# Performance work log

Hardware: AMD Instinct MI355X
Metric: run time of the kernel (lower is better)

## Reference

```python
import jax, jax.numpy as jnp
import numpy as np

STEPS = 100
RATE = 200
THR = 1.0
BETA = 0.0
SG_ALPHA = 2.0  # snntorch default ATan surrogate alpha


@jax.custom_vjp
def spike_fn(x):
    # heaviside spike with atan surrogate gradient (snntorch default)
    return (x > 0).astype(x.dtype)

def _spike_fwd(x):
    return spike_fn(x), x

def _spike_bwd(x, g):
    grad = (SG_ALPHA / 2.0) / (1.0 + (jnp.pi / 2.0 * SG_ALPHA * x) ** 2)
    return (g * grad,)

spike_fn.defvjp(_spike_fwd, _spike_bwd)


def conv2d(x, w):
    # x: [B,C,H,W], w: [O,I,K,K], VALID, stride 1, no bias
    return jax.lax.conv_general_dilated(
        x, w, window_strides=(1, 1), padding='VALID',
        dimension_numbers=('NCHW', 'OIHW', 'NCHW'))


def avg_pool2(x):
    s = jax.lax.reduce_window(x, 0.0, jax.lax.add, (1, 1, 2, 2), (1, 1, 2, 2), 'VALID')
    return s * 0.25


def lif(cur, mem):
    # snntorch Leaky, reset_mechanism='subtract'; reset signal is detached
    reset = jax.lax.stop_gradient((mem > THR).astype(cur.dtype))
    mem = BETA * mem + cur - reset * THR
    spk = spike_fn(mem - THR)
    return spk, mem


def setup_inputs() -> dict:
    key = jax.random.key(0)
    k1, k2, k3, k4 = jax.random.split(key, 4)
    B, C, H, W = 64, 3, 32, 32
    x = jax.random.uniform(k1, (B, C, H, W), dtype=jnp.float32)
    # kaiming-uniform-ish init scales (exact values irrelevant for correctness baseline)
    W_in = jax.random.normal(k2, (32, 3, 5, 5), dtype=jnp.float32) * 0.1
    W_h1 = jax.random.normal(k3, (64, 32, 5, 5), dtype=jnp.float32) * 0.05
    W_h2 = jax.random.normal(k4, (10, 1600), dtype=jnp.float32) * 0.02
    return {"x": x, "W_in": W_in, "W_h1": W_h1, "W_h2": W_h2}


def reference(x, W_in, W_h1, W_h2):
    B, C, H, W = x.shape
    K = W_in.shape[2]
    # poisson spike train: [steps, B, C, H, W]
    rescale = RATE / STEPS
    rand = jax.random.uniform(jax.random.key(1), (STEPS, B, C, H, W), dtype=x.dtype)
    spikes = (rand < x * rescale).astype(x.dtype)

    H1 = (H - K + 1) // 2; W1 = (W - K + 1) // 2           # after conv1+pool
    H2 = (H1 - K + 1) // 2; W2 = (W1 - K + 1) // 2          # after conv2+pool
    mem0 = (jnp.zeros((B, W_in.shape[0], H1, W1), x.dtype),
            jnp.zeros((B, W_h1.shape[0], H2, W2), x.dtype),
            jnp.zeros((B, W_h2.shape[0]), x.dtype))

    def step(carry, s):
        memin, memh1, memh2 = carry
        spkin, memin = lif(avg_pool2(conv2d(s, W_in)), memin)
        spkh1, memh1 = lif(avg_pool2(conv2d(spkin, W_h1)), memh1)
        flat = spkh1.reshape(spkh1.shape[0], -1)
        spkh2, memh2 = lif(flat @ W_h2.T, memh2)
        return (memin, memh1, memh2), (spkh2, memh2)

    _, (out_spikes, memh2_mem) = jax.lax.scan(step, mem0, spikes)
    return out_spikes, memh2_mem
```

## Files before the change

kernel.cpp:

```cpp
#include <hip/hip_runtime.h>
#include <stdint.h>


#define NSTEPS 100
#define NB 64
#define CAPF1 524288u
#define CAPF2 262144u

typedef short bf16x8 __attribute__((ext_vector_type(8)));
typedef float f32x4 __attribute__((ext_vector_type(4)));

__device__ __forceinline__ uint32_t rotl32(uint32_t v, uint32_t r) {
  return (v << r) | (v >> (32u - r));
}

__device__ __forceinline__ void threefry2x32(uint32_t k0, uint32_t k1,
                                             uint32_t& x0, uint32_t& x1) {
  uint32_t k2 = k0 ^ k1 ^ 0x1BD11BDAu;
  x0 += k0; x1 += k1;
#define TF_R(r) { x0 += x1; x1 = rotl32(x1, r); x1 ^= x0; }
  TF_R(13u) TF_R(15u) TF_R(26u) TF_R(6u)
  x0 += k1; x1 += k2 + 1u;
  TF_R(17u) TF_R(29u) TF_R(16u) TF_R(24u)
  x0 += k2; x1 += k0 + 2u;
  TF_R(13u) TF_R(15u) TF_R(26u) TF_R(6u)
  x0 += k0; x1 += k1 + 3u;
  TF_R(17u) TF_R(29u) TF_R(16u) TF_R(24u)
  x0 += k1; x1 += k2 + 4u;
  TF_R(13u) TF_R(15u) TF_R(26u) TF_R(6u)
  x0 += k2; x1 += k0 + 5u;
#undef TF_R
}

__device__ __forceinline__ double fold_pool_w(const float* W, int base, int pos) {
  int iy = pos / 6, ix = pos % 6;
  double w = 0.0;
  for (int dy = 0; dy < 2; ++dy) {
    int ky = iy - dy; if (ky < 0 || ky > 4) continue;
    for (int dx = 0; dx < 2; ++dx) {
      int kx = ix - dx; if (kx < 0 || kx > 4) continue;
      w += (double)W[base + ky * 5 + kx];
    }
  }
  return w;
}

__device__ __forceinline__ uint16_t f2bf(float x) {
  uint32_t u = __float_as_uint(x);
  uint32_t r = (u + 0x7fffu + ((u >> 16) & 1u)) >> 16;
  return (uint16_t)r;
}

__global__ __launch_bounds__(256) void prep_gen(const float* __restrict__ W_in,
                                                const float* __restrict__ W_h1,
                                                const float* __restrict__ x,
                                                double* __restrict__ W1R,
                                                double* __restrict__ W2R,
                                                uint16_t* __restrict__ WB1,
                                                uint16_t* __restrict__ WB2,
                                                float* __restrict__ EPS,
                                                uint32_t* __restrict__ cnt,
                                                uint32_t* __restrict__ rowm) {
  if (blockIdx.x >= 678) {
    int id = (blockIdx.x - 678) * 4 + (threadIdx.x >> 6);
    int lane = threadIdx.x & 63;
    int rp = id & 15, c = (id >> 4) % 3, tb = id / 48;
    int pix = rp * 64 + lane;
    int b = tb & 63;
    uint32_t i = (uint32_t)((tb * 3 + c) * 1024 + pix);
    uint32_t x0 = 0u, x1 = i;
    threefry2x32(0u, 1u, x0, x1);
    uint32_t bits = x0 ^ x1;
    float u = __uint_as_float((bits >> 9) | 0x3f800000u) - 1.0f;
    float xv = x[(b * 3 + c) * 1024 + pix];
    unsigned long long mask = __ballot(u < 2.0f * xv);
    if (lane == 0) ((unsigned long long*)rowm)[id] = mask;
    return;
  }
  if (blockIdx.x < 654) {
    int e = blockIdx.x * 256 + threadIdx.x;
    if (e < 3456) {
      int oj = e & 7, c = (e >> 3) % 3, pos = ((e >> 3) / 3) % 36, og = (e >> 3) / 108;
      int oc = og * 8 + oj;
      W1R[e] = fold_pool_w(W_in, (oc * 3 + c) * 25, pos);
    } else if (e < 77184) {
      int e2 = e - 3456;
      int oj = e2 & 15, pos = (e2 >> 4) % 36, c = ((e2 >> 4) / 36) % 32, og = e2 / 18432;
      int oc = og * 16 + oj;
      W2R[e2] = fold_pool_w(W_h1, (oc * 32 + c) * 25, pos);
    } else if (e < 93568) {
      int e3 = e - 77184;
      int j = e3 & 7, lane = (e3 >> 3) & 63, nt = (e3 >> 9) & 1, ks = (e3 >> 10) & 3, hl = e3 >> 12;
      int k = ks * 32 + (lane >> 4) * 8 + j;
      int oc = nt * 16 + (lane & 15);
      uint16_t val = 0;
      if (k < 108) {
        int c = k / 36, pos = k % 36;
        double w = fold_pool_w(W_in, (oc * 3 + c) * 25, pos);
        uint16_t hi = f2bf((float)w);
        if (hl == 0) val = hi;
        else {
          float hif = __uint_as_float(((uint32_t)hi) << 16);
          val = f2bf((float)(w - (double)hif));
        }
      }
      WB1[e3] = val;
    } else if (e < 167296) {
      int e4 = e - 93568;
      int j = e4 & 7, lane = (e4 >> 3) & 63, nt = (e4 >> 9) & 3, pos = e4 >> 11;
      int oc = nt * 16 + (lane & 15);
      int c  = (lane >> 4) * 8 + j;
      double w = fold_pool_w(W_h1, (oc * 32 + c) * 25, pos);
      uint16_t hi = f2bf((float)w);
      float hif = __uint_as_float(((uint32_t)hi) << 16);
      uint16_t lo = f2bf((float)(w - (double)hif));
      WB2[e4] = hi;
      WB2[73728 + e4] = lo;
    } else if (e < 167298) {
      cnt[e - 167296] = 0;
    }
  } else {
    int wid = threadIdx.x >> 6, lane = threadIdx.x & 63;
    int o = (blockIdx.x - 654) * 4 + wid;
    const double u24 = 5.9604644775390625e-08;
    double s = 0.0;
    if (o < 32) {
      for (int t = lane; t < 108; t += 64) {
        int pos = t / 3, c = t % 3;
        s += fabs(fold_pool_w(W_in, (o * 3 + c) * 25, pos));
      }
    } else {
      int oc = o - 32;
      for (int t = lane; t < 1152; t += 64) {
        int c = t / 36, pos = t % 36;
        s += fabs(fold_pool_w(W_h1, (oc * 32 + c) * 25, pos));
      }
    }
    #pragma unroll
    for (int off = 32; off > 0; off >>= 1) s += __shfl_xor(s, off);
    if (lane == 0)
      EPS[o] = (o < 32) ? (float)(s * (108.0 * u24 * 6.0) * 0.25)
                        : (float)(s * (1152.0 * u24 * 6.0) * 0.25);
  }
}

__global__ __launch_bounds__(256) void conv1_mfma(const uint32_t* __restrict__ rowm,
                                                  const uint16_t* __restrict__ WB1,
                                                  const float* __restrict__ EPS,
                                                  uint32_t* __restrict__ A1w,
                                                  uint32_t* __restrict__ B1w,
                                                  uint32_t* __restrict__ cnt,
                                                  uint32_t* __restrict__ list1) {
  __shared__ uint32_t sR[4][96];
  const int tid = threadIdx.x;
  const int wid = tid >> 6, lane = tid & 63;
  const int tb = blockIdx.x * 4 + wid;
  const int q = lane >> 4, ln = lane & 15;

  for (int i = lane; i < 96; i += 64) sR[wid][i] = rowm[tb * 96 + i];

  const float eps0 = EPS[ln];
  const float eps1 = EPS[16 + ln];

  bf16x8 bf[2][4][2];
  #pragma unroll
  for (int hl = 0; hl < 2; ++hl)
    #pragma unroll
    for (int ks = 0; ks < 4; ++ks)
      #pragma unroll
      for (int nt = 0; nt < 2; ++nt)
        bf[hl][ks][nt] =
            *(const bf16x8*)(WB1 + ((((hl * 4 + ks) * 2 + nt) * 64 + lane) * 8));

  const int wl = lane;
  const int qq = wl >> 2, rr = wl & 3;

  for (int mt = 0; mt < 13; ++mt) {
    int p = mt * 16 + ln;
    int pc = p < 196 ? p : 195;
    int oh = pc / 14, ow = pc % 14;
    uint64_t seg0 = 0, seg1 = 0, seg2 = 0;
    #pragma unroll
    for (int iy = 0; iy < 6; ++iy) {
      seg0 |= (uint64_t)((sR[wid][0 * 32 + 2 * oh + iy] >> (2 * ow)) & 0x3fu) << (6 * iy);
      seg1 |= (uint64_t)((sR[wid][1 * 32 + 2 * oh + iy] >> (2 * ow)) & 0x3fu) << (6 * iy);
      seg2 |= (uint64_t)((sR[wid][2 * 32 + 2 * oh + iy] >> (2 * ow)) & 0x3fu) << (6 * iy);
    }
    uint64_t lo = seg0 | (seg1 << 36);
    uint64_t hi = (seg1 >> 28) | (seg2 << 8);
    uint32_t wz[4] = {(uint32_t)lo, (uint32_t)(lo >> 32),
                      (uint32_t)hi, (uint32_t)(hi >> 32)};

    f32x4 acc0 = (f32x4)(0.0f), acc1 = (f32x4)(0.0f);
    #pragma unroll
    for (int ks = 0; ks < 4; ++ks) {
      uint32_t byte = (wz[ks] >> (q * 8)) & 0xffu;
      union { uint32_t u[4]; bf16x8 v; } a;
      #pragma unroll
      for (int i = 0; i < 4; ++i)
        a.u[i] = (((byte >> (2 * i)) & 1u) ? 0x3F80u : 0u) |
                 (((byte >> (2 * i + 1)) & 1u) ? 0x3F800000u : 0u);
      acc0 = __builtin_amdgcn_mfma_f32_16x16x32_bf16(a.v, bf[0][ks][0], acc0, 0, 0, 0);
      acc0 = __builtin_amdgcn_mfma_f32_16x16x32_bf16(a.v, bf[1][ks][0], acc0, 0, 0, 0);
      acc1 = __builtin_amdgcn_mfma_f32_16x16x32_bf16(a.v, bf[0][ks][1], acc1, 0, 0, 0);
      acc1 = __builtin_amdgcn_mfma_f32_16x16x32_bf16(a.v, bf[1][ks][1], acc1, 0, 0, 0);
    }

    unsigned long long bA0[4], bA1[4], bB0[4], bB1[4], bF0[4], bF1[4];
    #pragma unroll
    for (int r = 0; r < 4; ++r) {
      float c0 = acc0[r] * 0.25f;
      float c1 = acc1[r] * 0.25f;
      bA0[r] = __ballot(c0 > 1.0f);
      bB0[r] = __ballot(c0 > 2.0f);
      bF0[r] = __ballot(fabsf(c0 - 1.0f) <= eps0 || fabsf(c0 - 2.0f) <= eps0);
      bA1[r] = __ballot(c1 > 1.0f);
      bB1[r] = __ballot(c1 > 2.0f);
      bF1[r] = __ballot(fabsf(c1 - 1.0f) <= eps1 || fabsf(c1 - 2.0f) <= eps1);
    }

    int pw = mt * 16 + wl;
    if (wl < 16 && pw < 196) {
#define SEL(B) (rr == 0 ? B[0] : rr == 1 ? B[1] : rr == 2 ? B[2] : B[3])
      uint32_t wA = (uint32_t)((SEL(bA0) >> (qq * 16)) & 0xffffull) |
                    ((uint32_t)((SEL(bA1) >> (qq * 16)) & 0xffffull) << 16);
      uint32_t wB = (uint32_t)((SEL(bB0) >> (qq * 16)) & 0xffffull) |
                    ((uint32_t)((SEL(bB1) >> (qq * 16)) & 0xffffull) << 16);
      uint32_t wF = (uint32_t)((SEL(bF0) >> (qq * 16)) & 0xffffull) |
                    ((uint32_t)((SEL(bF1) >> (qq * 16)) & 0xffffull) << 16);
#undef SEL
      uint32_t idx = (uint32_t)(tb * 196 + pw);
      A1w[idx] = wA;
      B1w[idx] = wB;
      if (wF) {
        uint32_t n = (uint32_t)__popc(wF);
        uint32_t slot = atomicAdd(&cnt[0], n);
        uint32_t base = idx * 32u;
        while (wF) {
          int bit = __ffs(wF) - 1; wF &= wF - 1;
          if (slot < CAPF1) list1[slot] = base + (uint32_t)bit;
          ++slot;
        }
      }
    }
  }
}

__global__ __launch_bounds__(256) void fix1c(const uint32_t* __restrict__ cnt,
                                             const uint32_t* __restrict__ list,
                                             const uint32_t* __restrict__ rowm,
                                             const double* __restrict__ W1R,
                                             uint32_t* __restrict__ A1w,
                                             uint32_t* __restrict__ B1w) {
  uint32_t total = cnt[0]; if (total > CAPF1) total = CAPF1;
  const uint32_t g = blockIdx.x * 32 + (threadIdx.x >> 3);
  const int l = threadIdx.x & 7;
  const uint32_t gstride = gridDim.x * 32;
  for (uint32_t i = g; i < total; i += gstride) {
    uint32_t e = list[i];
    uint32_t x = e >> 5;
    int oc = (int)(e & 31u);
    int tb = (int)(x / 196), p = (int)(x % 196);
    int oh = p / 14, ow = p % 14;
    int og = oc >> 3, oj = oc & 7;
    const uint32_t* R = rowm + (size_t)tb * 96;
    double acc = 0.0;
    for (int t = l; t < 108; t += 8) {
      int pos = t / 3, c = t - pos * 3;
      int iy = pos / 6, ix = pos - iy * 6;
      double bd = (double)((R[c * 32 + 2 * oh + iy] >> (2 * ow + ix)) & 1u);
      acc = fma(bd, W1R[og * 864 + pos * 24 + c * 8 + oj], acc);
    }
    acc += __shfl_xor(acc, 1);
    acc += __shfl_xor(acc, 2);
    acc += __shfl_xor(acc, 4);
    if (l == 0) {
      float cur = (float)(acc * 0.25);
      uint32_t m = 1u << oc;
      if (cur > 1.0f) atomicOr(&A1w[x], m); else atomicAnd(&A1w[x], ~m);
      if (cur > 2.0f) atomicOr(&B1w[x], m); else atomicAnd(&B1w[x], ~m);
    }
  }
}

__global__ __launch_bounds__(64) void scan1(const uint32_t* __restrict__ A1w,
                                            const uint32_t* __restrict__ B1w,
                                            uint32_t* __restrict__ mask1) {
  int chain = blockIdx.x * 64 + threadIdx.x;
  if (chain >= NB * 196) return;
  int b = chain / 196, p = chain % 196;
  const size_t stride = (size_t)NB * 196;
  size_t base = (size_t)b * 196 + p;
  uint32_t prev = 0;
  #pragma unroll
  for (int seg = 0; seg < 4; ++seg) {
    uint32_t Abuf[25], Bbuf[25];
    size_t sb = base + (size_t)(seg * 25) * stride;
    #pragma unroll
    for (int i = 0; i < 25; ++i) {
      Abuf[i] = A1w[sb + i * stride];
      Bbuf[i] = B1w[sb + i * stride];
    }
    #pragma unroll
    for (int i = 0; i < 25; ++i) {
      uint32_t s = (Abuf[i] & ~prev) | (Bbuf[i] & prev);
      mask1[sb + i * stride] = s;
      prev = s;
    }
  }
}

#define CONV2_EPILOG(ACC, TBV)                                                \
  {                                                                           \
    const int w = lane;                                                       \
    const int pw = w >> 1, hfw = w & 1;                                       \
    _Pragma("unroll")                                                         \
    for (int mt2 = 0; mt2 < 2; ++mt2) {                                       \
      const int pt = pw - mt2 * 16;                                           \
      const bool wvalid = (w < 50) && (pt >= 0) && (pt < 16) && (pw < 25);    \
      const int qw = (pt & 15) >> 2, rw = pt & 3;                             \
      uint32_t wA = 0, wB = 0, wF = 0;                                        \
      _Pragma("unroll")                                                       \
      for (int nt = 0; nt < 4; ++nt) {                                        \
        unsigned long long bA[4], bB[4], bF[4];                               \
        _Pragma("unroll")                                                     \
        for (int reg = 0; reg < 4; ++reg) {                                   \
          float c = ACC[mt2 * 4 + nt][reg] * 0.25f;                           \
          float e = epsv[nt];                                                 \
          bA[reg] = __ballot(c > 1.0f);                                       \
          bB[reg] = __ballot(c > 2.0f);                                       \
          bF[reg] = __ballot(fabsf(c - 1.0f) <= e || fabsf(c - 2.0f) <= e);   \
        }                                                                     \
        if (wvalid && (nt >> 1) == hfw) {                                     \
          const int sh = (nt & 1) * 16;                                       \
          unsigned long long sA = rw == 0 ? bA[0] : rw == 1 ? bA[1] : rw == 2 ? bA[2] : bA[3]; \
          unsigned long long sB = rw == 0 ? bB[0] : rw == 1 ? bB[1] : rw == 2 ? bB[2] : bB[3]; \
          unsigned long long sF = rw == 0 ? bF[0] : rw == 1 ? bF[1] : rw == 2 ? bF[2] : bF[3]; \
          wA |= (uint32_t)((sA >> (qw * 16)) & 0xffffull) << sh;              \
          wB |= (uint32_t)((sB >> (qw * 16)) & 0xffffull) << sh;              \
          wF |= (uint32_t)((sF >> (qw * 16)) & 0xffffull) << sh;              \
        }                                                                     \
      }                                                                       \
      if (wvalid) {                                                           \
        uint32_t idx = (uint32_t)((TBV) * 25 + pw) * 2 + hfw;                 \
        A2w[idx] = wA;                                                        \
        B2w[idx] = wB;                                                        \
        if (wF) {                                                             \
          uint32_t n = (uint32_t)__popc(wF);                                  \
          uint32_t slot = atomicAdd(&cnt[1], n);                              \
          uint32_t base2 = idx * 32u;                                         \
          while (wF) {                                                        \
            int bit = __ffs(wF) - 1; wF &= wF - 1;                            \
            if (slot < CAPF2) list2[slot] = base2 + (uint32_t)bit;            \
            ++slot;                                                           \
          }                                                                   \
        }                                                                     \
      }                                                                       \
    }                                                                         \
  }

__global__ __launch_bounds__(256, 3) void conv2_mfma(const uint32_t* __restrict__ mask1,
                                                     const uint16_t* __restrict__ WB,
                                                     const float* __restrict__ EPS,
                                                     uint32_t* __restrict__ A2w,
                                                     uint32_t* __restrict__ B2w,
                                                     uint32_t* __restrict__ cnt,
                                                     uint32_t* __restrict__ list2) {
  __shared__ uint32_t sM[8 * 196];
  const int tid = threadIdx.x;
  const int wid = tid >> 6, lane = tid & 63;
  const int tb0 = blockIdx.x * 8 + wid * 2;

  for (int i = lane; i < 392; i += 64)
    sM[wid * 392 + i] = mask1[(size_t)tb0 * 196 + i];

  const int q  = lane >> 4;
  const int ln = lane & 15;
  float epsv[4];
  #pragma unroll
  for (int nt = 0; nt < 4; ++nt) epsv[nt] = EPS[32 + nt * 16 + ln];

  const int p0 = ln;
  const int p1 = 16 + ln;
  const bool v1 = (p1 < 25);
  const int oh0 = p0 / 5, ow0 = p0 % 5;
  const int p1c = v1 ? p1 : 0;
  const int oh1 = p1c / 5, ow1 = p1c % 5;

  f32x4 accA[8], accB[8];
  #pragma unroll
  for (int i = 0; i < 8; ++i) { accA[i] = (f32x4)(0.0f); accB[i] = (f32x4)(0.0f); }

  const uint32_t* sW0 = &sM[wid * 392];
  const uint32_t* sW1 = sW0 + 196;

  for (int iy = 0; iy < 6; ++iy) {
    #pragma unroll
    for (int ix = 0; ix < 6; ++ix) {
      const int pos = iy * 6 + ix;
      const int o0 = (2 * oh0 + iy) * 14 + 2 * ow0 + ix;
      const int o1 = (2 * oh1 + iy) * 14 + 2 * ow1 + ix;
      uint32_t w00 = sW0[o0];
      uint32_t w01 = v1 ? sW0[o1] : 0u;
      uint32_t w10 = sW1[o0];
      uint32_t w11 = v1 ? sW1[o1] : 0u;
      uint32_t b00 = (w00 >> (q * 8)) & 0xffu;
      uint32_t b01 = (w01 >> (q * 8)) & 0xffu;
      uint32_t b10 = (w10 >> (q * 8)) & 0xffu;
      uint32_t b11 = (w11 >> (q * 8)) & 0xffu;
      union { uint32_t u[4]; bf16x8 v; } a00, a01, a10, a11;
      #pragma unroll
      for (int i = 0; i < 4; ++i) {
        a00.u[i] = (((b00 >> (2 * i)) & 1u) ? 0x3F80u : 0u) |
                   (((b00 >> (2 * i + 1)) & 1u) ? 0x3F800000u : 0u);
        a01.u[i] = (((b01 >> (2 * i)) & 1u) ? 0x3F80u : 0u) |
                   (((b01 >> (2 * i + 1)) & 1u) ? 0x3F800000u : 0u);
        a10.u[i] = (((b10 >> (2 * i)) & 1u) ? 0x3F80u : 0u) |
                   (((b10 >> (2 * i + 1)) & 1u) ? 0x3F800000u : 0u);
        a11.u[i] = (((b11 >> (2 * i)) & 1u) ? 0x3F80u : 0u) |
                   (((b11 >> (2 * i + 1)) & 1u) ? 0x3F800000u : 0u);
      }
      const uint16_t* bhi_base = WB + (size_t)pos * 2048 + lane * 8;
      const uint16_t* blo_base = bhi_base + 73728;
      #pragma unroll
      for (int nt = 0; nt < 4; ++nt) {
        bf16x8 bhi = *(const bf16x8*)(bhi_base + nt * 512);
        bf16x8 blo = *(const bf16x8*)(blo_base + nt * 512);
        accA[nt] = __builtin_amdgcn_mfma_f32_16x16x32_bf16(a00.v, bhi, accA[nt], 0, 0, 0);
        accA[nt] = __builtin_amdgcn_mfma_f32_16x16x32_bf16(a00.v, blo, accA[nt], 0, 0, 0);
        accA[4 + nt] = __builtin_amdgcn_mfma_f32_16x16x32_bf16(a01.v, bhi, accA[4 + nt], 0, 0, 0);
        accA[4 + nt] = __builtin_amdgcn_mfma_f32_16x16x32_bf16(a01.v, blo, accA[4 + nt], 0, 0, 0);
        accB[nt] = __builtin_amdgcn_mfma_f32_16x16x32_bf16(a10.v, bhi, accB[nt], 0, 0, 0);
        accB[nt] = __builtin_amdgcn_mfma_f32_16x16x32_bf16(a10.v, blo, accB[nt], 0, 0, 0);
        accB[4 + nt] = __builtin_amdgcn_mfma_f32_16x16x32_bf16(a11.v, bhi, accB[4 + nt], 0, 0, 0);
        accB[4 + nt] = __builtin_amdgcn_mfma_f32_16x16x32_bf16(a11.v, blo, accB[4 + nt], 0, 0, 0);
      }
    }
  }

  CONV2_EPILOG(accA, tb0)
  CONV2_EPILOG(accB, (tb0 + 1))
}

__global__ __launch_bounds__(256) void fix2c(const uint32_t* __restrict__ cnt,
                                             const uint32_t* __restrict__ list,
                                             const uint32_t* __restrict__ mask1,
                                             const double* __restrict__ W2R,
                                             uint32_t* __restrict__ A2w,
                                             uint32_t* __restrict__ B2w) {
  uint32_t total = cnt[1]; if (total > CAPF2) total = CAPF2;
  const uint32_t g = blockIdx.x * 16 + (threadIdx.x >> 4);
  const int l = threadIdx.x & 15;
  const uint32_t gstride = gridDim.x * 16;
  for (uint32_t i = g; i < total; i += gstride) {
    uint32_t e = list[i];
    uint32_t wi = e >> 5;
    int bit = (int)(e & 31u);
    uint32_t x = wi >> 1;
    int oc = (int)((wi & 1u) * 32u) + bit;
    int tb = (int)(x / 25), p = (int)(x % 25);
    int oh = p / 5, ow = p % 5;
    int og = oc >> 4, oj = oc & 15;
    const uint32_t* M = mask1 + (size_t)tb * 196;
    double acc = 0.0;
    for (int t = l; t < 1152; t += 16) {
      int c = t / 36, pos = t - c * 36;
      int iy = pos / 6, ix = pos - iy * 6;
      uint32_t mm = M[(2 * oh + iy) * 14 + 2 * ow + ix];
      double bd = (double)((mm >> c) & 1u);
      acc = fma(bd, W2R[og * 18432 + c * 576 + pos * 16 + oj], acc);
    }
    acc += __shfl_xor(acc, 1);
    acc += __shfl_xor(acc, 2);
    acc += __shfl_xor(acc, 4);
    acc += __shfl_xor(acc, 8);
    if (l == 0) {
      float cur = (float)(acc * 0.25);
      uint32_t m = 1u << bit;
      if (cur > 1.0f) atomicOr(&A2w[wi], m); else atomicAnd(&A2w[wi], ~m);
      if (cur > 2.0f) atomicOr(&B2w[wi], m); else atomicAnd(&B2w[wi], ~m);
    }
  }
}

__global__ __launch_bounds__(64) void scan2(const uint64_t* __restrict__ A2q,
                                            const uint64_t* __restrict__ B2q,
                                            uint64_t* __restrict__ mask2) {
  int chain = blockIdx.x * 64 + threadIdx.x;
  if (chain >= NB * 25) return;
  int b = chain / 25, p = chain % 25;
  const size_t stride = (size_t)NB * 25;
  size_t base = (size_t)b * 25 + p;
  uint64_t prev = 0;
  #pragma unroll
  for (int seg = 0; seg < 4; ++seg) {
    uint64_t Abuf[25], Bbuf[25];
    size_t sb = base + (size_t)(seg * 25) * stride;
    #pragma unroll
    for (int i = 0; i < 25; ++i) {
      Abuf[i] = A2q[sb + i * stride];
      Bbuf[i] = B2q[sb + i * stride];
    }
    #pragma unroll
    for (int i = 0; i < 25; ++i) {
      uint64_t s = (Abuf[i] & ~prev) | (Bbuf[i] & prev);
      mask2[sb + i * stride] = s;
      prev = s;
    }
  }
}

__global__ __launch_bounds__(256) void fc_kernel(const uint64_t* __restrict__ mask2,
                                                 const float* __restrict__ W2,
                                                 float* __restrict__ cur3) {
  int gid = blockIdx.x * 256 + threadIdx.x;
  if (gid >= NSTEPS * NB * 80) return;
  int tb = gid / 80, r = gid % 80;
  int o = r >> 3, s = r & 7;
  const uint64_t* m = mask2 + (size_t)tb * 25;
  const float* w = W2 + o * 1600 + s * 200;

  uint64_t mw[25];
  #pragma unroll
  for (int p = 0; p < 25; ++p) mw[p] = m[p];

  const int oc0 = s * 8;
  double acc0 = 0.0, acc1 = 0.0;
  #pragma unroll
  for (int j = 0; j < 8; ++j) {
    const float* wj = w + j * 25;
    double a = 0.0;
    #pragma unroll
    for (int p = 0; p < 25; ++p) {
      double bd = (double)((mw[p] >> (oc0 + j)) & 1ull);
      a = fma(bd, (double)wj[p], a);
    }
    if (j & 1) acc1 += a; else acc0 += a;
  }
  double acc = acc0 + acc1;
  acc += __shfl_xor(acc, 4);
  acc += __shfl_xor(acc, 2);
  acc += __shfl_xor(acc, 1);
  if (s == 0) cur3[tb * 10 + o] = (float)acc;
}

__global__ __launch_bounds__(64) void lif3_kernel(const float* __restrict__ cur3,
                                                  float* __restrict__ out) {
  int bo = blockIdx.x * 64 + threadIdx.x;
  if (bo >= NB * 10) return;
  float prev = 0.0f;
  #pragma unroll
  for (int seg = 0; seg < 4; ++seg) {
    float cbuf[25];
    #pragma unroll
    for (int i = 0; i < 25; ++i) cbuf[i] = cur3[(seg * 25 + i) * 640 + bo];
    #pragma unroll
    for (int i = 0; i < 25; ++i) {
      int t = seg * 25 + i;
      float mem = cbuf[i] - prev;
      bool s = mem > 1.0f;
      out[t * 640 + bo] = s ? 1.0f : 0.0f;
      out[NSTEPS * 640 + t * 640 + bo] = mem;
      prev = s ? 1.0f : 0.0f;
    }
  }
}

extern "C" void kernel_launch(void* const* d_in, const int* in_sizes, int n_in,
                              void* d_out, int out_size, void* d_ws, size_t ws_size,
                              hipStream_t stream) {
  const float* x    = (const float*)d_in[0];
  const float* W_in = (const float*)d_in[1];
  const float* W_h1 = (const float*)d_in[2];
  const float* W_h2 = (const float*)d_in[3];
  float* out = (float*)d_out;

  unsigned char* ws = (unsigned char*)d_ws;
  double*   W1R   = (double*)(ws + 0);
  double*   W2R   = (double*)(ws + 27648);
  uint16_t* WB1   = (uint16_t*)(ws + 617472);
  uint16_t* WB2   = (uint16_t*)(ws + 650240);
  float*    EPS   = (float*)(ws + 945152);
  uint32_t* cnt   = (uint32_t*)(ws + 945536);
  uint32_t* rowm  = (uint32_t*)(ws + 945664);
  uint32_t* A1w   = (uint32_t*)(ws + 3403264);
  uint32_t* B1w   = (uint32_t*)(ws + 8420864);
  uint32_t* mask1 = (uint32_t*)(ws + 13438464);
  uint32_t* A2w   = (uint32_t*)(ws + 18456064);
  uint32_t* B2w   = (uint32_t*)(ws + 19736064);
  uint64_t* mask2 = (uint64_t*)(ws + 21016064);
  float*    cur3  = (float*)(ws + 22296064);
  uint32_t* list1 = (uint32_t*)(ws + 22552064);
  uint32_t* list2 = (uint32_t*)(ws + 24649216);

  prep_gen<<<678 + 76800, 256, 0, stream>>>(W_in, W_h1, x, W1R, W2R, WB1, WB2,
                                            EPS, cnt, rowm);
  conv1_mfma<<<1600, 256, 0, stream>>>(rowm, WB1, EPS, A1w, B1w, cnt, list1);
  fix1c<<<1024, 256, 0, stream>>>(cnt, list1, rowm, W1R, A1w, B1w);
  scan1<<<(NB * 196 + 63) / 64, 64, 0, stream>>>(A1w, B1w, mask1);
  conv2_mfma<<<800, 256, 0, stream>>>(mask1, WB2, EPS, A2w, B2w, cnt, list2);
  fix2c<<<1024, 256, 0, stream>>>(cnt, list2, mask1, W2R, A2w, B2w);
  scan2<<<(NB * 25 + 63) / 64, 64, 0, stream>>>((const uint64_t*)A2w,
                                                (const uint64_t*)B2w, mask2);
  fc_kernel<<<(NSTEPS * NB * 80 + 255) / 256, 256, 0, stream>>>(mask2, W_h2, cur3);
  lif3_kernel<<<10, 64, 0, stream>>>(cur3, out);
}
```

Baseline: 299.3 us.

## Fuse pipeline stages into one cooperative persistent kernel with grid syncs

```diff
diff --git a/kernel.cpp b/kernel.cpp
--- a/kernel.cpp
+++ b/kernel.cpp
@@ -1,6 +1,9 @@
 #include <hip/hip_runtime.h>
+#include <hip/hip_cooperative_groups.h>
 #include <stdint.h>
 
+
+namespace cg = cooperative_groups;
 
 #define NSTEPS 100
 #define NB 64
@@ -9,6 +12,38 @@
 
 typedef short bf16x8 __attribute__((ext_vector_type(8)));
 typedef float f32x4 __attribute__((ext_vector_type(4)));
+
+struct Ptrs {
+  double *W1R, *W2R;
+  uint16_t *WB1, *WB2;
+  float *EPS;
+  uint32_t *cnt, *rowm, *A1w, *B1w, *mask1, *A2w, *B2w;
+  uint64_t *mask2;
+  float *cur3;
+  uint32_t *list1, *list2;
+};
+
+__device__ __forceinline__ Ptrs mk(void* wsv) {
+  unsigned char* ws = (unsigned char*)wsv;
+  Ptrs p;
+  p.W1R   = (double*)(ws + 0);
+  p.W2R   = (double*)(ws + 27648);
+  p.WB1   = (uint16_t*)(ws + 617472);
+  p.WB2   = (uint16_t*)(ws + 650240);
+  p.EPS   = (float*)(ws + 945152);
+  p.cnt   = (uint32_t*)(ws + 945536);
+  p.rowm  = (uint32_t*)(ws + 945664);
+  p.A1w   = (uint32_t*)(ws + 3403264);
+  p.B1w   = (uint32_t*)(ws + 8420864);
+  p.mask1 = (uint32_t*)(ws + 13438464);
+  p.A2w   = (uint32_t*)(ws + 18456064);
+  p.B2w   = (uint32_t*)(ws + 19736064);
+  p.mask2 = (uint64_t*)(ws + 21016064);
+  p.cur3  = (float*)(ws + 22296064);
+  p.list1 = (uint32_t*)(ws + 22552064);
+  p.list2 = (uint32_t*)(ws + 24649216);
+  return p;
+}
 
 __device__ __forceinline__ uint32_t rotl32(uint32_t v, uint32_t r) {
   return (v << r) | (v >> (32u - r));
@@ -51,18 +86,10 @@
   return (uint16_t)r;
 }
 
-__global__ __launch_bounds__(256) void prep_gen(const float* __restrict__ W_in,
-                                                const float* __restrict__ W_h1,
-                                                const float* __restrict__ x,
-                                                double* __restrict__ W1R,
-                                                double* __restrict__ W2R,
-                                                uint16_t* __restrict__ WB1,
-                                                uint16_t* __restrict__ WB2,
-                                                float* __restrict__ EPS,
-                                                uint32_t* __restrict__ cnt,
-                                                uint32_t* __restrict__ rowm) {
-  if (blockIdx.x >= 678) {
-    int id = (blockIdx.x - 678) * 4 + (threadIdx.x >> 6);
+__device__ void st_prep(int v, const float* W_in, const float* W_h1,
+                        const float* x, const Ptrs& P) {
+  if (v >= 678) {
+    int id = (v - 678) * 4 + (threadIdx.x >> 6);
     int lane = threadIdx.x & 63;
     int rp = id & 15, c = (id >> 4) % 3, tb = id / 48;
     int pix = rp * 64 + lane;
@@ -74,20 +101,20 @@
     float u = __uint_as_float((bits >> 9) | 0x3f800000u) - 1.0f;
     float xv = x[(b * 3 + c) * 1024 + pix];
     unsigned long long mask = __ballot(u < 2.0f * xv);
-    if (lane == 0) ((unsigned long long*)rowm)[id] = mask;
+    if (lane == 0) ((unsigned long long*)P.rowm)[id] = mask;
     return;
   }
-  if (blockIdx.x < 654) {
-    int e = blockIdx.x * 256 + threadIdx.x;
+  if (v < 654) {
+    int e = v * 256 + threadIdx.x;
     if (e < 3456) {
       int oj = e & 7, c = (e >> 3) % 3, pos = ((e >> 3) / 3) % 36, og = (e >> 3) / 108;
       int oc = og * 8 + oj;
-      W1R[e] = fold_pool_w(W_in, (oc * 3 + c) * 25, pos);
+      P.W1R[e] = fold_pool_w(W_in, (oc * 3 + c) * 25, pos);
     } else if (e < 77184) {
       int e2 = e - 3456;
       int oj = e2 & 15, pos = (e2 >> 4) % 36, c = ((e2 >> 4) / 36) % 32, og = e2 / 18432;
       int oc = og * 16 + oj;
-      W2R[e2] = fold_pool_w(W_h1, (oc * 32 + c) * 25, pos);
+      P.W2R[e2] = fold_pool_w(W_h1, (oc * 32 + c) * 25, pos);
     } else if (e < 93568) {
       int e3 = e - 77184;
       int j = e3 & 7, lane = (e3 >> 3) & 63, nt = (e3 >> 9) & 1, ks = (e3 >> 10) & 3, hl = e3 >> 12;
@@ -104,7 +131,7 @@
           val = f2bf((float)(w - (double)hif));
         }
       }
-      WB1[e3] = val;
+      P.WB1[e3] = val;
     } else if (e < 167296) {
       int e4 = e - 93568;
       int j = e4 & 7, lane = (e4 >> 3) & 63, nt = (e4 >> 9) & 3, pos = e4 >> 11;
@@ -114,14 +141,14 @@
       uint16_t hi = f2bf((float)w);
       float hif = __uint_as_float(((uint32_t)hi) << 16);
       uint16_t lo = f2bf((float)(w - (double)hif));
-      WB2[e4] = hi;
-      WB2[73728 + e4] = lo;
+      P.WB2[e4] = hi;
+      P.WB2[73728 + e4] = lo;
     } else if (e < 167298) {
-      cnt[e - 167296] = 0;
+      P.cnt[e - 167296] = 0;
     }
   } else {
     int wid = threadIdx.x >> 6, lane = threadIdx.x & 63;
-    int o = (blockIdx.x - 654) * 4 + wid;
+    int o = (v - 654) * 4 + wid;
     const double u24 = 5.9604644775390625e-08;
     double s = 0.0;
     if (o < 32) {
@@ -139,28 +166,23 @@
     #pragma unroll
     for (int off = 32; off > 0; off >>= 1) s += __shfl_xor(s, off);
     if (lane == 0)
-      EPS[o] = (o < 32) ? (float)(s * (108.0 * u24 * 6.0) * 0.25)
-                        : (float)(s * (1152.0 * u24 * 6.0) * 0.25);
-  }
-}
-
-__global__ __launch_bounds__(256) void conv1_mfma(const uint32_t* __restrict__ rowm,
-                                                  const uint16_t* __restrict__ WB1,
-                                                  const float* __restrict__ EPS,
-                                                  uint32_t* __restrict__ A1w,
-                                                  uint32_t* __restrict__ B1w,
-                                                  uint32_t* __restrict__ cnt,
-                                                  uint32_t* __restrict__ list1) {
-  __shared__ uint32_t sR[4][96];
+      P.EPS[o] = (o < 32) ? (float)(s * (108.0 * u24 * 6.0) * 0.25)
+                          : (float)(s * (1152.0 * u24 * 6.0) * 0.25);
+  }
+}
+
+__device__ void st_conv1(int g, const Ptrs& P, uint32_t* sR ) {
+  uint32_t* cnt = P.cnt;
+  uint32_t* list1 = P.list1;
   const int tid = threadIdx.x;
   const int wid = tid >> 6, lane = tid & 63;
-  const int tb = blockIdx.x * 4 + wid;
+  const int tb = g * 4 + wid;
   const int q = lane >> 4, ln = lane & 15;
 
-  for (int i = lane; i < 96; i += 64) sR[wid][i] = rowm[tb * 96 + i];
-
-  const float eps0 = EPS[ln];
-  const float eps1 = EPS[16 + ln];
+  for (int i = lane; i < 96; i += 64) sR[wid * 96 + i] = P.rowm[tb * 96 + i];
+
+  const float eps0 = P.EPS[ln];
+  const float eps1 = P.EPS[16 + ln];
 
   bf16x8 bf[2][4][2];
   #pragma unroll
@@ -170,7 +192,7 @@
       #pragma unroll
       for (int nt = 0; nt < 2; ++nt)
         bf[hl][ks][nt] =
-            *(const bf16x8*)(WB1 + ((((hl * 4 + ks) * 2 + nt) * 64 + lane) * 8));
+            *(const bf16x8*)(P.WB1 + ((((hl * 4 + ks) * 2 + nt) * 64 + lane) * 8));
 
   const int wl = lane;
   const int qq = wl >> 2, rr = wl & 3;
@@ -182,9 +204,9 @@
     uint64_t seg0 = 0, seg1 = 0, seg2 = 0;
     #pragma unroll
     for (int iy = 0; iy < 6; ++iy) {
-      seg0 |= (uint64_t)((sR[wid][0 * 32 + 2 * oh + iy] >> (2 * ow)) & 0x3fu) << (6 * iy);
-      seg1 |= (uint64_t)((sR[wid][1 * 32 + 2 * oh + iy] >> (2 * ow)) & 0x3fu) << (6 * iy);
-      seg2 |= (uint64_t)((sR[wid][2 * 32 + 2 * oh + iy] >> (2 * ow)) & 0x3fu) << (6 * iy);
+      seg0 |= (uint64_t)((sR[wid * 96 + 0 * 32 + 2 * oh + iy] >> (2 * ow)) & 0x3fu) << (6 * iy);
+      seg1 |= (uint64_t)((sR[wid * 96 + 1 * 32 + 2 * oh + iy] >> (2 * ow)) & 0x3fu) << (6 * iy);
+      seg2 |= (uint64_t)((sR[wid * 96 + 2 * 32 + 2 * oh + iy] >> (2 * ow)) & 0x3fu) << (6 * iy);
     }
     uint64_t lo = seg0 | (seg1 << 36);
     uint64_t hi = (seg1 >> 28) | (seg2 << 8);
@@ -230,8 +252,8 @@
                     ((uint32_t)((SEL(bF1) >> (qq * 16)) & 0xffffull) << 16);
 #undef SEL
       uint32_t idx = (uint32_t)(tb * 196 + pw);
-      A1w[idx] = wA;
-      B1w[idx] = wB;
+      P.A1w[idx] = wA;
+      P.B1w[idx] = wB;
       if (wF) {
         uint32_t n = (uint32_t)__popc(wF);
         uint32_t slot = atomicAdd(&cnt[0], n);
@@ -246,30 +268,25 @@
   }
 }
 
-__global__ __launch_bounds__(256) void fix1c(const uint32_t* __restrict__ cnt,
-                                             const uint32_t* __restrict__ list,
-                                             const uint32_t* __restrict__ rowm,
-                                             const double* __restrict__ W1R,
-                                             uint32_t* __restrict__ A1w,
-                                             uint32_t* __restrict__ B1w) {
-  uint32_t total = cnt[0]; if (total > CAPF1) total = CAPF1;
+__device__ void st_fix1(const Ptrs& P) {
+  uint32_t total = P.cnt[0]; if (total > CAPF1) total = CAPF1;
   const uint32_t g = blockIdx.x * 32 + (threadIdx.x >> 3);
   const int l = threadIdx.x & 7;
   const uint32_t gstride = gridDim.x * 32;
   for (uint32_t i = g; i < total; i += gstride) {
-    uint32_t e = list[i];
+    uint32_t e = P.list1[i];
     uint32_t x = e >> 5;
     int oc = (int)(e & 31u);
     int tb = (int)(x / 196), p = (int)(x % 196);
     int oh = p / 14, ow = p % 14;
     int og = oc >> 3, oj = oc & 7;
-    const uint32_t* R = rowm + (size_t)tb * 96;
+    const uint32_t* R = P.rowm + (size_t)tb * 96;
     double acc = 0.0;
     for (int t = l; t < 108; t += 8) {
       int pos = t / 3, c = t - pos * 3;
       int iy = pos / 6, ix = pos - iy * 6;
       double bd = (double)((R[c * 32 + 2 * oh + iy] >> (2 * ow + ix)) & 1u);
-      acc = fma(bd, W1R[og * 864 + pos * 24 + c * 8 + oj], acc);
+      acc = fma(bd, P.W1R[og * 864 + pos * 24 + c * 8 + oj], acc);
     }
     acc += __shfl_xor(acc, 1);
     acc += __shfl_xor(acc, 2);
@@ -277,16 +294,14 @@
     if (l == 0) {
       float cur = (float)(acc * 0.25);
       uint32_t m = 1u << oc;
-      if (cur > 1.0f) atomicOr(&A1w[x], m); else atomicAnd(&A1w[x], ~m);
-      if (cur > 2.0f) atomicOr(&B1w[x], m); else atomicAnd(&B1w[x], ~m);
-    }
-  }
-}
-
-__global__ __launch_bounds__(64) void scan1(const uint32_t* __restrict__ A1w,
-                                            const uint32_t* __restrict__ B1w,
-                                            uint32_t* __restrict__ mask1) {
-  int chain = blockIdx.x * 64 + threadIdx.x;
+      if (cur > 1.0f) atomicOr(&P.A1w[x], m); else atomicAnd(&P.A1w[x], ~m);
+      if (cur > 2.0f) atomicOr(&P.B1w[x], m); else atomicAnd(&P.B1w[x], ~m);
+    }
+  }
+}
+
+__device__ void st_scan1(int v, const Ptrs& P) {
+  int chain = v * 256 + threadIdx.x;
   if (chain >= NB * 196) return;
   int b = chain / 196, p = chain % 196;
   const size_t stride = (size_t)NB * 196;
@@ -298,13 +313,13 @@
     size_t sb = base + (size_t)(seg * 25) * stride;
     #pragma unroll
     for (int i = 0; i < 25; ++i) {
-      Abuf[i] = A1w[sb + i * stride];
-      Bbuf[i] = B1w[sb + i * stride];
+      Abuf[i] = P.A1w[sb + i * stride];
+      Bbuf[i] = P.B1w[sb + i * stride];
     }
     #pragma unroll
     for (int i = 0; i < 25; ++i) {
       uint32_t s = (Abuf[i] & ~prev) | (Bbuf[i] & prev);
-      mask1[sb + i * stride] = s;
+      P.mask1[sb + i * stride] = s;
       prev = s;
     }
   }
@@ -343,15 +358,15 @@
       }                                                                       \
       if (wvalid) {                                                           \
         uint32_t idx = (uint32_t)((TBV) * 25 + pw) * 2 + hfw;                 \
-        A2w[idx] = wA;                                                        \
-        B2w[idx] = wB;                                                        \
+        P.A2w[idx] = wA;                                                      \
+        P.B2w[idx] = wB;                                                      \
         if (wF) {                                                             \
           uint32_t n = (uint32_t)__popc(wF);                                  \
-          uint32_t slot = atomicAdd(&cnt[1], n);                              \
+          uint32_t slot = atomicAdd(&P.cnt[1], n);                            \
           uint32_t base2 = idx * 32u;                                         \
           while (wF) {                                                        \
             int bit = __ffs(wF) - 1; wF &= wF - 1;                            \
-            if (slot < CAPF2) list2[slot] = base2 + (uint32_t)bit;            \
+            if (slot < CAPF2) P.list2[slot] = base2 + (uint32_t)bit;          \
             ++slot;                                                           \
           }                                                                   \
         }                                                                     \
@@ -359,26 +374,20 @@
     }                                                                         \
   }
 
-__global__ __launch_bounds__(256, 3) void conv2_mfma(const uint32_t* __restrict__ mask1,
-                                                     const uint16_t* __restrict__ WB,
-                                                     const float* __restrict__ EPS,
-                                                     uint32_t* __restrict__ A2w,
-                                                     uint32_t* __restrict__ B2w,
-                                                     uint32_t* __restrict__ cnt,
-                                                     uint32_t* __restrict__ list2) {
-  __shared__ uint32_t sM[8 * 196];
+__device__ void st_conv2(int g, const Ptrs& P, uint32_t* sM ,
+                         uint16_t* sWB ) {
   const int tid = threadIdx.x;
   const int wid = tid >> 6, lane = tid & 63;
-  const int tb0 = blockIdx.x * 8 + wid * 2;
+  const int tb0 = g * 8 + wid * 2;
 
   for (int i = lane; i < 392; i += 64)
-    sM[wid * 392 + i] = mask1[(size_t)tb0 * 196 + i];
+    sM[wid * 392 + i] = P.mask1[(size_t)tb0 * 196 + i];
 
   const int q  = lane >> 4;
   const int ln = lane & 15;
   float epsv[4];
   #pragma unroll
-  for (int nt = 0; nt < 4; ++nt) epsv[nt] = EPS[32 + nt * 16 + ln];
+  for (int nt = 0; nt < 4; ++nt) epsv[nt] = P.EPS[32 + nt * 16 + ln];
 
   const int p0 = ln;
   const int p1 = 16 + ln;
@@ -393,11 +402,17 @@
 
   const uint32_t* sW0 = &sM[wid * 392];
   const uint32_t* sW1 = sW0 + 196;
+  const uint4* wbsrc = (const uint4*)P.WB2;
 
   for (int iy = 0; iy < 6; ++iy) {
     #pragma unroll
     for (int ix = 0; ix < 6; ++ix) {
       const int pos = iy * 6 + ix;
+      __syncthreads();
+      ((uint4*)sWB)[tid]       = wbsrc[pos * 256 + tid];
+      ((uint4*)sWB)[tid + 256] = wbsrc[9216 + pos * 256 + tid];
+      __syncthreads();
+
       const int o0 = (2 * oh0 + iy) * 14 + 2 * ow0 + ix;
       const int o1 = (2 * oh1 + iy) * 14 + 2 * ow1 + ix;
       uint32_t w00 = sW0[o0];
@@ -420,12 +435,10 @@
         a11.u[i] = (((b11 >> (2 * i)) & 1u) ? 0x3F80u : 0u) |
                    (((b11 >> (2 * i + 1)) & 1u) ? 0x3F800000u : 0u);
       }
-      const uint16_t* bhi_base = WB + (size_t)pos * 2048 + lane * 8;
-      const uint16_t* blo_base = bhi_base + 73728;
       #pragma unroll
       for (int nt = 0; nt < 4; ++nt) {
-        bf16x8 bhi = *(const bf16x8*)(bhi_base + nt * 512);
-        bf16x8 blo = *(const bf16x8*)(blo_base + nt * 512);
+        bf16x8 bhi = *(const bf16x8*)(sWB + (nt * 64 + lane) * 8);
+        bf16x8 blo = *(const bf16x8*)(sWB + 2048 + (nt * 64 + lane) * 8);
         accA[nt] = __builtin_amdgcn_mfma_f32_16x16x32_bf16(a00.v, bhi, accA[nt], 0, 0, 0);
         accA[nt] = __builtin_amdgcn_mfma_f32_16x16x32_bf16(a00.v, blo, accA[nt], 0, 0, 0);
         accA[4 + nt] = __builtin_amdgcn_mfma_f32_16x16x32_bf16(a01.v, bhi, accA[4 + nt], 0, 0, 0);
@@ -442,18 +455,13 @@
   CONV2_EPILOG(accB, (tb0 + 1))
 }
 
-__global__ __launch_bounds__(256) void fix2c(const uint32_t* __restrict__ cnt,
-                                             const uint32_t* __restrict__ list,
-                                             const uint32_t* __restrict__ mask1,
-                                             const double* __restrict__ W2R,
-                                             uint32_t* __restrict__ A2w,
-                                             uint32_t* __restrict__ B2w) {
-  uint32_t total = cnt[1]; if (total > CAPF2) total = CAPF2;
+__device__ void st_fix2(const Ptrs& P) {
+  uint32_t total = P.cnt[1]; if (total > CAPF2) total = CAPF2;
   const uint32_t g = blockIdx.x * 16 + (threadIdx.x >> 4);
   const int l = threadIdx.x & 15;
   const uint32_t gstride = gridDim.x * 16;
   for (uint32_t i = g; i < total; i += gstride) {
-    uint32_t e = list[i];
+    uint32_t e = P.list2[i];
     uint32_t wi = e >> 5;
     int bit = (int)(e & 31u);
     uint32_t x = wi >> 1;
@@ -461,14 +469,14 @@
     int tb = (int)(x / 25), p = (int)(x % 25);
     int oh = p / 5, ow = p % 5;
     int og = oc >> 4, oj = oc & 15;
-    const uint32_t* M = mask1 + (size_t)tb * 196;
+    const uint32_t* M = P.mask1 + (size_t)tb * 196;
     double acc = 0.0;
     for (int t = l; t < 1152; t += 16) {
       int c = t / 36, pos = t - c * 36;
       int iy = pos / 6, ix = pos - iy * 6;
       uint32_t mm = M[(2 * oh + iy) * 14 + 2 * ow + ix];
       double bd = (double)((mm >> c) & 1u);
-      acc = fma(bd, W2R[og * 18432 + c * 576 + pos * 16 + oj], acc);
+      acc = fma(bd, P.W2R[og * 18432 + c * 576 + pos * 16 + oj], acc);
     }
     acc += __shfl_xor(acc, 1);
     acc += __shfl_xor(acc, 2);
@@ -477,17 +485,17 @@
     if (l == 0) {
       float cur = (float)(acc * 0.25);
       uint32_t m = 1u << bit;
-      if (cur > 1.0f) atomicOr(&A2w[wi], m); else atomicAnd(&A2w[wi], ~m);
-      if (cur > 2.0f) atomicOr(&B2w[wi], m); else atomicAnd(&B2w[wi], ~m);
-    }
-  }
-}
-
-__global__ __launch_bounds__(64) void scan2(const uint64_t* __restrict__ A2q,
-                                            const uint64_t* __restrict__ B2q,
-                                            uint64_t* __restrict__ mask2) {
-  int chain = blockIdx.x * 64 + threadIdx.x;
+      if (cur > 1.0f) atomicOr(&P.A2w[wi], m); else atomicAnd(&P.A2w[wi], ~m);
+      if (cur > 2.0f) atomicOr(&P.B2w[wi], m); else atomicAnd(&P.B2w[wi], ~m);
+    }
+  }
+}
+
+__device__ void st_scan2(int v, const Ptrs& P) {
+  int chain = v * 256 + threadIdx.x;
   if (chain >= NB * 25) return;
+  const uint64_t* A2q = (const uint64_t*)P.A2w;
+  const uint64_t* B2q = (const uint64_t*)P.B2w;
   int b = chain / 25, p = chain % 25;
   const size_t stride = (size_t)NB * 25;
   size_t base = (size_t)b * 25 + p;
@@ -504,56 +512,52 @@
     #pragma unroll
     for (int i = 0; i < 25; ++i) {
       uint64_t s = (Abuf[i] & ~prev) | (Bbuf[i] & prev);
-      mask2[sb + i * stride] = s;
+      P.mask2[sb + i * stride] = s;
       prev = s;
     }
   }
 }
 
-__global__ __launch_bounds__(256) void fc_kernel(const uint64_t* __restrict__ mask2,
-                                                 const float* __restrict__ W2,
-                                                 float* __restrict__ cur3) {
-  int gid = blockIdx.x * 256 + threadIdx.x;
-  if (gid >= NSTEPS * NB * 80) return;
-  int tb = gid / 80, r = gid % 80;
-  int o = r >> 3, s = r & 7;
-  const uint64_t* m = mask2 + (size_t)tb * 25;
-  const float* w = W2 + o * 1600 + s * 200;
-
-  uint64_t mw[25];
-  #pragma unroll
-  for (int p = 0; p < 25; ++p) mw[p] = m[p];
-
-  const int oc0 = s * 8;
-  double acc0 = 0.0, acc1 = 0.0;
-  #pragma unroll
-  for (int j = 0; j < 8; ++j) {
-    const float* wj = w + j * 25;
-    double a = 0.0;
-    #pragma unroll
-    for (int p = 0; p < 25; ++p) {
-      double bd = (double)((mw[p] >> (oc0 + j)) & 1ull);
-      a = fma(bd, (double)wj[p], a);
-    }
-    if (j & 1) acc1 += a; else acc0 += a;
-  }
-  double acc = acc0 + acc1;
-  acc += __shfl_xor(acc, 4);
-  acc += __shfl_xor(acc, 2);
-  acc += __shfl_xor(acc, 1);
-  if (s == 0) cur3[tb * 10 + o] = (float)acc;
-}
-
-__global__ __launch_bounds__(64) void lif3_kernel(const float* __restrict__ cur3,
-                                                  float* __restrict__ out) {
-  int bo = blockIdx.x * 64 + threadIdx.x;
+__device__ void st_fc(const Ptrs& P, const float* W2) {
+  for (int gid = blockIdx.x * 256 + threadIdx.x; gid < NSTEPS * NB * 80;
+       gid += gridDim.x * 256) {
+    int tb = gid / 80, r = gid % 80;
+    int o = r >> 3, s = r & 7;
+    const uint64_t* m = P.mask2 + (size_t)tb * 25;
+    const float* w = W2 + o * 1600 + s * 200;
+    uint64_t mw[25];
+    #pragma unroll
+    for (int p = 0; p < 25; ++p) mw[p] = m[p];
+    const int oc0 = s * 8;
+    double acc0 = 0.0, acc1 = 0.0;
+    #pragma unroll
+    for (int j = 0; j < 8; ++j) {
+      const float* wj = w + j * 25;
+      double a = 0.0;
+      #pragma unroll
+      for (int p = 0; p < 25; ++p) {
+        double bd = (double)((mw[p] >> (oc0 + j)) & 1ull);
+        a = fma(bd, (double)wj[p], a);
+      }
+      if (j & 1) acc1 += a; else acc0 += a;
+    }
+    double acc = acc0 + acc1;
+    acc += __shfl_xor(acc, 4);
+    acc += __shfl_xor(acc, 2);
+    acc += __shfl_xor(acc, 1);
+    if (s == 0) P.cur3[tb * 10 + o] = (float)acc;
+  }
+}
+
+__device__ void st_lif3(int v, const Ptrs& P, float* out) {
+  int bo = v * 256 + threadIdx.x;
   if (bo >= NB * 10) return;
   float prev = 0.0f;
   #pragma unroll
   for (int seg = 0; seg < 4; ++seg) {
     float cbuf[25];
     #pragma unroll
-    for (int i = 0; i < 25; ++i) cbuf[i] = cur3[(seg * 25 + i) * 640 + bo];
+    for (int i = 0; i < 25; ++i) cbuf[i] = P.cur3[(seg * 25 + i) * 640 + bo];
     #pragma unroll
     for (int i = 0; i < 25; ++i) {
       int t = seg * 25 + i;
@@ -564,6 +568,76 @@
       prev = s ? 1.0f : 0.0f;
     }
   }
+}
+
+__global__ __launch_bounds__(256, 3) void snn_mega(const float* x, const float* W_in,
+                                                   const float* W_h1, const float* W_h2,
+                                                   float* out, void* wsv) {
+  Ptrs P = mk(wsv);
+  cg::grid_group grid = cg::this_grid();
+  __shared__ __align__(16) char smem[14464];
+  uint32_t* sR  = (uint32_t*)smem;
+  uint32_t* sM  = (uint32_t*)smem;
+  uint16_t* sWB = (uint16_t*)(smem + 6272);
+  const int nb = gridDim.x;
+
+  for (int v = blockIdx.x; v < 678 + 76800; v += nb) st_prep(v, W_in, W_h1, x, P);
+  grid.sync();
+  for (int g = blockIdx.x; g < 1600; g += nb) st_conv1(g, P, sR);
+  grid.sync();
+  st_fix1(P);
+  grid.sync();
+  for (int v = blockIdx.x; v < 49; v += nb) st_scan1(v, P);
+  grid.sync();
+  for (int g = blockIdx.x; g < 800; g += nb) st_conv2(g, P, sM, sWB);
+  grid.sync();
+  st_fix2(P);
+  grid.sync();
+  for (int v = blockIdx.x; v < 7; v += nb) st_scan2(v, P);
+  grid.sync();
+  st_fc(P, W_h2);
+  grid.sync();
+  for (int v = blockIdx.x; v < 3; v += nb) st_lif3(v, P, out);
+}
+
+__global__ __launch_bounds__(256) void k_prep(const float* x, const float* W_in,
+                                              const float* W_h1, void* wsv) {
+  Ptrs P = mk(wsv);
+  st_prep(blockIdx.x, W_in, W_h1, x, P);
+}
+__global__ __launch_bounds__(256) void k_conv1(void* wsv) {
+  Ptrs P = mk(wsv);
+  __shared__ __align__(16) uint32_t sR[4 * 96];
+  st_conv1(blockIdx.x, P, sR);
+}
+__global__ __launch_bounds__(256) void k_fix1(void* wsv) {
+  Ptrs P = mk(wsv);
+  st_fix1(P);
+}
+__global__ __launch_bounds__(256) void k_scan1(void* wsv) {
+  Ptrs P = mk(wsv);
+  st_scan1(blockIdx.x, P);
+}
+__global__ __launch_bounds__(256, 3) void k_conv2(void* wsv) {
+  Ptrs P = mk(wsv);
+  __shared__ __align__(16) char smem[14464];
+  st_conv2(blockIdx.x, P, (uint32_t*)smem, (uint16_t*)(smem + 6272));
+}
+__global__ __launch_bounds__(256) void k_fix2(void* wsv) {
+  Ptrs P = mk(wsv);
+  st_fix2(P);
+}
+__global__ __launch_bounds__(256) void k_scan2(void* wsv) {
+  Ptrs P = mk(wsv);
+  st_scan2(blockIdx.x, P);
+}
+__global__ __launch_bounds__(256) void k_fc(const float* W_h2, void* wsv) {
+  Ptrs P = mk(wsv);
+  st_fc(P, W_h2);
+}
+__global__ __launch_bounds__(256) void k_lif3(float* out, void* wsv) {
+  Ptrs P = mk(wsv);
+  st_lif3(blockIdx.x, P, out);
 }
 
 extern "C" void kernel_launch(void* const* d_in, const int* in_sizes, int n_in,
@@ -574,34 +648,29 @@
   const float* W_h1 = (const float*)d_in[2];
   const float* W_h2 = (const float*)d_in[3];
   float* out = (float*)d_out;
-
-  unsigned char* ws = (unsigned char*)d_ws;
-  double*   W1R   = (double*)(ws + 0);
-  double*   W2R   = (double*)(ws + 27648);
-  uint16_t* WB1   = (uint16_t*)(ws + 617472);
-  uint16_t* WB2   = (uint16_t*)(ws + 650240);
-  float*    EPS   = (float*)(ws + 945152);
-  uint32_t* cnt   = (uint32_t*)(ws + 945536);
-  uint32_t* rowm  = (uint32_t*)(ws + 945664);
-  uint32_t* A1w   = (uint32_t*)(ws + 3403264);
-  uint32_t* B1w   = (uint32_t*)(ws + 8420864);
-  uint32_t* mask1 = (uint32_t*)(ws + 13438464);
-  uint32_t* A2w   = (uint32_t*)(ws + 18456064);
-  uint32_t* B2w   = (uint32_t*)(ws + 19736064);
-  uint64_t* mask2 = (uint64_t*)(ws + 21016064);
-  float*    cur3  = (float*)(ws + 22296064);
-  uint32_t* list1 = (uint32_t*)(ws + 22552064);
-  uint32_t* list2 = (uint32_t*)(ws + 24649216);
-
-  prep_gen<<<678 + 76800, 256, 0, stream>>>(W_in, W_h1, x, W1R, W2R, WB1, WB2,
-                                            EPS, cnt, rowm);
-  conv1_mfma<<<1600, 256, 0, stream>>>(rowm, WB1, EPS, A1w, B1w, cnt, list1);
-  fix1c<<<1024, 256, 0, stream>>>(cnt, list1, rowm, W1R, A1w, B1w);
-  scan1<<<(NB * 196 + 63) / 64, 64, 0, stream>>>(A1w, B1w, mask1);
-  conv2_mfma<<<800, 256, 0, stream>>>(mask1, WB2, EPS, A2w, B2w, cnt, list2);
-  fix2c<<<1024, 256, 0, stream>>>(cnt, list2, mask1, W2R, A2w, B2w);
-  scan2<<<(NB * 25 + 63) / 64, 64, 0, stream>>>((const uint64_t*)A2w,
-                                                (const uint64_t*)B2w, mask2);
-  fc_kernel<<<(NSTEPS * NB * 80 + 255) / 256, 256, 0, stream>>>(mask2, W_h2, cur3);
-  lif3_kernel<<<10, 64, 0, stream>>>(cur3, out);
-}
+  void* wsv = d_ws;
+
+  bool coop_ok = false;
+  int maxb = 0;
+  hipError_t occ = hipOccupancyMaxActiveBlocksPerMultiprocessor(&maxb, snn_mega, 256, (size_t)0);
+  if (occ == hipSuccess && maxb >= 1) {
+    int nblk = maxb * 256;
+    if (nblk > 2048) nblk = 2048;
+    void* args[] = {(void*)&x, (void*)&W_in, (void*)&W_h1, (void*)&W_h2,
+                    (void*)&out, (void*)&wsv};
+    hipError_t e = hipLaunchCooperativeKernel(snn_mega, dim3(nblk), dim3(256),
+                                              args, 0u, stream);
+    coop_ok = (e == hipSuccess);
+  }
+  if (!coop_ok) {
+    k_prep<<<678 + 76800, 256, 0, stream>>>(x, W_in, W_h1, wsv);
+    k_conv1<<<1600, 256, 0, stream>>>(wsv);
+    k_fix1<<<1024, 256, 0, stream>>>(wsv);
+    k_scan1<<<49, 256, 0, stream>>>(wsv);
+    k_conv2<<<800, 256, 0, stream>>>(wsv);
+    k_fix2<<<1024, 256, 0, stream>>>(wsv);
+    k_scan2<<<7, 256, 0, stream>>>(wsv);
+    k_fc<<<2000, 256, 0, stream>>>(W_h2, wsv);
+    k_lif3<<<3, 256, 0, stream>>>(out, wsv);
+  }
+}
```

Measured after the change: 664.0 us. 2.22x slower.
